# Performance work log

Hardware: AMD Instinct MI355X
Metric: run time of the kernel (lower is better)

## Reference

```python
import jax, jax.numpy as jnp
import numpy as np

VOXEL_SIZE = (0.2, 0.2, 4.0)
BN_EPS = 1e-3
N_PILLARS, MAX_PTS, IN_CH, OUT_CH = 100000, 32, 4, 64


def setup_inputs() -> dict:
    key = jax.random.key(0)
    k0, k1, k2, k3, k4 = jax.random.split(key, 5)
    features = jax.random.normal(k0, (N_PILLARS, MAX_PTS, IN_CH), dtype=jnp.float32)
    num_points = jax.random.randint(k1, (N_PILLARS,), 1, MAX_PTS + 1).astype(jnp.int32)
    batch = jax.random.randint(k2, (N_PILLARS, 1), 0, 4)
    z = jnp.zeros((N_PILLARS, 1), dtype=jnp.int32)
    yx = jax.random.randint(k3, (N_PILLARS, 2), 0, 512)
    coors = jnp.concatenate([batch, z, yx], axis=1).astype(jnp.int32)  # (b, z, y, x)
    # PFN params: Linear(10 -> 64, no bias, kaiming), BN affine
    W = jax.random.normal(k4, (IN_CH + 6, OUT_CH), dtype=jnp.float32) * np.sqrt(2.0 / (IN_CH + 6))
    gamma = jnp.ones((OUT_CH,), dtype=jnp.float32)
    beta = jnp.zeros((OUT_CH,), dtype=jnp.float32)
    return {"features": features, "W": W, "gamma": gamma, "beta": beta,
            "num_points": num_points, "coors": coors}


def reference(features, W, gamma, beta, num_points, coors):
    # features: [N, P, 4]; coors: [N, 4] (batch, z, y, x)
    vs = jnp.asarray(VOXEL_SIZE, dtype=features.dtype)
    P = features.shape[1]
    xyz = features[..., :3]  # [N, P, 3]
    # padding indicator: point j of pillar i is valid iff j < num_points[i]
    maskf = (jnp.arange(P)[None, :] < num_points[:, None]).astype(features.dtype)[..., None]  # [N,P,1]
    # cluster center: masked mean of xyz per pillar, broadcast back to points
    cnt = jnp.maximum(num_points, 1).astype(features.dtype)[:, None]
    voxel_mean = (xyz * maskf).sum(axis=1) / cnt  # [N, 3]
    f_cluster = xyz - voxel_mean[:, None, :]
    # voxel center offset (faithful to source: coors[:, 1:] * voxel_size + 0.5*voxel_size)
    voxel_center = (coors[:, 1:].astype(features.dtype) + 0.5) * vs  # [N, 3]
    f_center = xyz - voxel_center[:, None, :]
    feats = jnp.concatenate([features, f_cluster, f_center], axis=-1) * maskf  # [N, P, 10]
    # PFN layer: Linear -> BatchNorm (training stats over all points, per channel) -> ReLU
    h = jnp.einsum('npc,cd->npd', feats, W)  # [N, P, 64]
    mu = h.mean(axis=(0, 1))
    var = h.var(axis=(0, 1))
    h = (h - mu) * jax.lax.rsqrt(var + BN_EPS) * gamma + beta
    h = jax.nn.relu(h)
    # dynamic_scatter with mode='max': max-reduce points within each pillar
    voxel_feats = h.max(axis=1)  # [N, 64]
    return voxel_feats
```

## Files before the change

kernel.cpp:

```cpp
#include <hip/hip_runtime.h>
#include <stdint.h>

#define NP 100000
#define MP 32
#define OC 64
#define NBLK 1563
#define BNEPS 0.001f
#define MTOT 3200000.0
#define GIDX(i,j) ((i)*10 - (i)*((i)-1)/2 + ((j)-(i)))
#define BG(a,b) B[((a)<=(b)) ? ((a)*(7-(a))/2+(b)) : ((b)*(7-(b))/2+(a))]

typedef float f2 __attribute__((ext_vector_type(2)));

__device__ __forceinline__ float redall(float v) {
    v += __int_as_float(__builtin_amdgcn_update_dpp(0, __float_as_int(v), 0xB1,  0xF, 0xF, true));
    v += __int_as_float(__builtin_amdgcn_update_dpp(0, __float_as_int(v), 0x4E,  0xF, 0xF, true));
    v += __int_as_float(__builtin_amdgcn_update_dpp(0, __float_as_int(v), 0x141, 0xF, 0xF, true));
    v += __int_as_float(__builtin_amdgcn_update_dpp(0, __float_as_int(v), 0x140, 0xF, 0xF, true));
    v += __int_as_float(__builtin_amdgcn_ds_swizzle(__float_as_int(v), 0x401F));
    v += __shfl_xor(v, 32, 64);
    return v;
}

__global__ void sap_prep(const float* __restrict__ W, const float* __restrict__ gamma,
                         float* __restrict__ wptab, float4* __restrict__ btab)
{
    const int c = threadIdx.x;
    float w2[4], wcl[3], wce[3];
    w2[3] = W[3 * OC + c];
    #pragma unroll
    for (int k = 0; k < 3; ++k) {
        wcl[k] = W[(4 + k) * OC + c];
        wce[k] = W[(7 + k) * OC + c];
        w2[k]  = W[k * OC + c] + wcl[k] + wce[k];
    }
    const float sgn = (gamma[c] >= 0.0f) ? 1.0f : -1.0f;
    #pragma unroll
    for (int k = 0; k < 4; ++k)
        wptab[(((c >> 1) * 4) + k) * 2 + (c & 1)] = w2[k] * sgn;
    btab[2*c]   = make_float4(wcl[0]*sgn, wcl[1]*sgn, wcl[2]*sgn, wce[0]*sgn);
    btab[2*c+1] = make_float4(wce[1]*sgn, wce[2]*sgn, sgn, 0.0f);
}

__global__ __launch_bounds__(256, 4) void sap_pass1(
    const float4* __restrict__ feat4, const int* __restrict__ nump,
    const int4* __restrict__ coors4, const f2* __restrict__ wptab,
    const float4* __restrict__ btab, float* __restrict__ hsel,
    float* __restrict__ partials)
{
    const int lane = threadIdx.x & 63;
    const int swid = __builtin_amdgcn_readfirstlane(threadIdx.x >> 6);
    const int n = blockIdx.x * 64 + lane;
    const bool valid = n < NP;
    const int nn = valid ? n : NP - 1;
    const int cnt = valid ? nump[nn] : 0;
    const int4 cr = coors4[nn];
    const float cenz = ((float)cr.y + 0.5f) * 0.2f;
    const float ceny = ((float)cr.z + 0.5f) * 0.2f;
    const float cenx = ((float)cr.w + 0.5f) * 4.0f;
    const float4* __restrict__ fp = feat4 + (size_t)nn * MP;

    f2 wA[8], wB[8], wC[8], wD[8];
    #pragma unroll
    for (int j = 0; j < 8; ++j) {
        const int base = (swid * 8 + j) * 4;
        wA[j] = wptab[base];     wB[j] = wptab[base + 1];
        wC[j] = wptab[base + 2]; wD[j] = wptab[base + 3];
    }

    f2 mac[8];
    #pragma unroll
    for (int j = 0; j < 8; ++j) mac[j] = (f2){-3.0e38f, -3.0e38f};
    float S0 = 0.f, S1 = 0.f, S2 = 0.f, S3 = 0.f;
    float B[10];
    #pragma unroll
    for (int k = 0; k < 10; ++k) B[k] = 0.f;
    const bool doB = (swid == 0);

#define POINT(FF, P) {                                                          \
    const bool act = (P) < cnt;                                                 \
    const float neg = act ? 0.0f : -3.0e38f;                                    \
    const f2 neg2 = {neg, neg};                                                 \
    const f2 fx = {(FF).x, (FF).x}, fy = {(FF).y, (FF).y};                      \
    const f2 fz = {(FF).z, (FF).z}, fw = {(FF).w, (FF).w};                      \
    _Pragma("unroll")                                                           \
    for (int j = 0; j < 8; ++j) {                                               \
        const f2 d = __builtin_elementwise_fma(fx, wA[j],                       \
                     __builtin_elementwise_fma(fy, wB[j],                       \
                     __builtin_elementwise_fma(fz, wC[j],                       \
                     __builtin_elementwise_fma(fw, wD[j], neg2))));             \
        mac[j] = __builtin_elementwise_max(mac[j], d);                          \
    }                                                                           \
    const float ax = act ? (FF).x : 0.0f, ay = act ? (FF).y : 0.0f;             \
    const float az = act ? (FF).z : 0.0f;                                       \
    S0 += ax; S1 += ay; S2 += az;                                               \
    if (doB) {                                                                  \
        const float aw = act ? (FF).w : 0.0f;                                   \
        S3 += aw;                                                               \
        B[0]=fmaf(ax,ax,B[0]); B[1]=fmaf(ax,ay,B[1]); B[2]=fmaf(ax,az,B[2]);    \
        B[3]=fmaf(ax,aw,B[3]); B[4]=fmaf(ay,ay,B[4]); B[5]=fmaf(ay,az,B[5]);    \
        B[6]=fmaf(ay,aw,B[6]); B[7]=fmaf(az,az,B[7]); B[8]=fmaf(az,aw,B[8]);    \
        B[9]=fmaf(aw,aw,B[9]);                                                  \
    } }

    {
        float4 b0 = fp[0], b1 = fp[1], b2 = fp[2], b3 = fp[3];
        #pragma unroll 1
        for (int pq = 0; pq < 8; ++pq) {
            const int pb = pq * 4;
            float4 n0 = b0, n1 = b1, n2 = b2, n3 = b3;
            if (pq < 7) { n0 = fp[pb+4]; n1 = fp[pb+5]; n2 = fp[pb+6]; n3 = fp[pb+7]; }
            POINT(b0, pb + 0) POINT(b1, pb + 1)
            POINT(b2, pb + 2) POINT(b3, pb + 3)
            b0 = n0; b1 = n1; b2 = n2; b3 = n3;
        }
    }
#undef POINT

    const float fcnt = (float)cnt;
    const float rc = __builtin_amdgcn_rcpf(fmaxf(fcnt, 1.0f));
    const float mx = S0 * rc, my = S1 * rc, mz = S2 * rc;
    const float fl = (cnt < MP) ? 0.0f : -3.0e38f;
    #pragma unroll
    for (int q = 0; q < 4; ++q) {
        float o[4];
        #pragma unroll
        for (int k = 0; k < 4; ++k) {
            const int cc = q * 4 + k;
            const int c = swid * 16 + cc;
            const float4 bA = btab[2 * c];
            const float4 bB = btab[2 * c + 1];
            const float bias = -(mx * bA.x + my * bA.y + mz * bA.z
                               + cenz * bA.w + ceny * bB.x + cenx * bB.y);
            const float m = (cc & 1) ? mac[cc >> 1].y : mac[cc >> 1].x;
            o[k] = bB.z * fmaxf(m + bias, fl);
        }
        if (valid)
            *reinterpret_cast<float4*>(hsel + (size_t)n * OC + swid * 16 + q * 4)
                = make_float4(o[0], o[1], o[2], o[3]);
    }

    if (doB) {
        float vals[62];
        const float Sf[4] = {S0, S1, S2, S3};
        const float mu[3] = {S0 * rc, S1 * rc, S2 * rc};
        const float ce[3] = {cenz, ceny, cenx};
        #pragma unroll
        for (int i = 0; i < 4; ++i)
            #pragma unroll
            for (int j = i; j < 4; ++j)
                vals[GIDX(i, j)] = BG(i, j);
        #pragma unroll
        for (int i = 0; i < 4; ++i)
            #pragma unroll
            for (int t = 0; t < 3; ++t)
                vals[GIDX(i, 4 + t)] = BG(i, t) - mu[t] * Sf[i];
        #pragma unroll
        for (int s = 0; s < 3; ++s)
            #pragma unroll
            for (int t = s; t < 3; ++t)
                vals[GIDX(4 + s, 4 + t)] = BG(s, t) - mu[s] * Sf[t];
        #pragma unroll
        for (int i = 0; i < 4; ++i)
            #pragma unroll
            for (int t = 0; t < 3; ++t)
                vals[GIDX(i, 7 + t)] = BG(i, t) - ce[t] * Sf[i];
        #pragma unroll
        for (int s = 0; s < 3; ++s)
            #pragma unroll
            for (int t = 0; t < 3; ++t)
                vals[GIDX(4 + s, 7 + t)] = BG(s, t) - mu[s] * Sf[t];
        #pragma unroll
        for (int s = 0; s < 3; ++s)
            #pragma unroll
            for (int t = s; t < 3; ++t)
                vals[GIDX(7 + s, 7 + t)] =
                    fmaf(fcnt * ce[s], ce[t], BG(s, t) - ce[s] * Sf[t] - ce[t] * Sf[s]);
        vals[55] = S0; vals[56] = S1; vals[57] = S2; vals[58] = S3;
        vals[59] = fmaf(-fcnt, cenz, S0);
        vals[60] = fmaf(-fcnt, ceny, S1);
        vals[61] = fmaf(-fcnt, cenx, S2);

        #pragma unroll
        for (int k = 0; k < 62; ++k) vals[k] = redall(vals[k]);
        float mine = 0.0f;
        #pragma unroll
        for (int k = 0; k < 62; ++k) mine = (lane == k) ? vals[k] : mine;
        if (lane < 62)
            partials[(size_t)blockIdx.x * 64 + lane] = mine;
    }
}

__global__ __launch_bounds__(256) void sap_reduce1(const float* __restrict__ partials,
                                                   float* __restrict__ partials2)
{
    __shared__ float acc[4][64];
    const int k = threadIdx.x & 63, q = threadIdx.x >> 6;
    const int g = blockIdx.x;
    float s = 0.0f;
    for (int b = g + 64 * q; b < NBLK; b += 256)
        s += partials[(size_t)b * 64 + k];
    acc[q][k] = s;
    __syncthreads();
    if (threadIdx.x < 64)
        partials2[(size_t)g * 64 + threadIdx.x] =
            (acc[0][threadIdx.x] + acc[1][threadIdx.x]) +
            (acc[2][threadIdx.x] + acc[3][threadIdx.x]);
}

__global__ void sap_finalize(const float* __restrict__ partials2,
                             const float* __restrict__ W,
                             const float* __restrict__ gamma,
                             const float* __restrict__ beta,
                             float* __restrict__ scsh)
{
    __shared__ float acc[4][64];
    __shared__ float stats[64];
    const int tid = threadIdx.x;
    const int k = tid & 63, q = tid >> 6;
    float s = 0.0f;
    #pragma unroll
    for (int i = 0; i < 16; ++i)
        s += partials2[(size_t)(q + 4 * i) * 64 + k];
    acc[q][k] = s;
    __syncthreads();
    if (tid < 64) stats[tid] = (acc[0][tid] + acc[1][tid]) + (acc[2][tid] + acc[3][tid]);
    __syncthreads();
    if (tid >= 64) return;
    const int c = tid;
    double G[55];
    #pragma unroll
    for (int kk = 0; kk < 55; ++kk) G[kk] = (double)stats[kk];
    double Sg[10];
    Sg[0] = (double)stats[55]; Sg[1] = (double)stats[56];
    Sg[2] = (double)stats[57]; Sg[3] = (double)stats[58];
    Sg[4] = 0.0; Sg[5] = 0.0; Sg[6] = 0.0;
    Sg[7] = (double)stats[59]; Sg[8] = (double)stats[60]; Sg[9] = (double)stats[61];
    double w[10];
    #pragma unroll
    for (int kk = 0; kk < 10; ++kk) w[kk] = (double)W[kk * OC + c];
    double sh = 0.0, qq = 0.0;
    #pragma unroll
    for (int kk = 0; kk < 10; ++kk) sh += Sg[kk] * w[kk];
    for (int i = 0; i < 10; ++i)
        for (int j = i; j < 10; ++j) {
            const double t = w[i] * w[j] * G[GIDX(i, j)];
            qq += (i == j) ? t : 2.0 * t;
        }
    const double mu_d = sh / MTOT;
    const double var_d = qq / MTOT - mu_d * mu_d;
    const float sc = gamma[c] * rsqrtf((float)var_d + BNEPS);
    scsh[c]      = sc;
    scsh[64 + c] = beta[c] - (float)mu_d * sc;
}

__global__ __launch_bounds__(256) void sap_pass2(const float* __restrict__ scsh,
                                                 float* __restrict__ out)
{
    const int idx = blockIdx.x * 256 + threadIdx.x;
    if (idx >= (NP * OC) / 4) return;
    float4 h = reinterpret_cast<float4*>(out)[idx];
    const int ci = idx & 15;
    const float4 sc = reinterpret_cast<const float4*>(scsh)[ci];
    const float4 sh = reinterpret_cast<const float4*>(scsh + 64)[ci];
    float4 o;
    o.x = fmaxf(fmaf(h.x, sc.x, sh.x), 0.0f);
    o.y = fmaxf(fmaf(h.y, sc.y, sh.y), 0.0f);
    o.z = fmaxf(fmaf(h.z, sc.z, sh.z), 0.0f);
    o.w = fmaxf(fmaf(h.w, sc.w, sh.w), 0.0f);
    reinterpret_cast<float4*>(out)[idx] = o;
}

extern "C" void kernel_launch(void* const* d_in, const int* in_sizes, int n_in,
                              void* d_out, int out_size, void* d_ws, size_t ws_size,
                              hipStream_t stream) {
    const float* feat  = (const float*)d_in[0];
    const float* W     = (const float*)d_in[1];
    const float* gamma = (const float*)d_in[2];
    const float* beta  = (const float*)d_in[3];
    const int*   nump  = (const int*)d_in[4];
    const int*   coors = (const int*)d_in[5];
    float* out = (float*)d_out;

    float* wptab = (float*)d_ws;
    float4* btab = (float4*)((char*)d_ws + 1024);
    float* scsh  = (float*)((char*)d_ws + 3072);
    float* partials  = (float*)((char*)d_ws + 4096);
    float* partials2 = (float*)((char*)d_ws + 4096 + 1563*64*4);

    sap_prep<<<1, 64, 0, stream>>>(W, gamma, wptab, btab);
    sap_pass1<<<NBLK, 256, 0, stream>>>(
        (const float4*)feat, nump, (const int4*)coors, (const f2*)wptab,
        btab, out, partials);
    sap_reduce1<<<64, 256, 0, stream>>>(partials, partials2);
    sap_finalize<<<1, 256, 0, stream>>>(partials2, W, gamma, beta, scsh);
    sap_pass2<<<(NP * OC / 4 + 255) / 256, 256, 0, stream>>>(scsh, out);
}
```

Before: 60.57 us.

## Stage pillar features into LDS via direct global-to-LDS loads with XOR swizzle

Each block cooperatively copies its 64 pillars' point features into shared memory using direct global-to-LDS loads with a swizzled layout, then every wave reads points from LDS instead of global memory. This removes the fourfold redundant global/L1 traffic from the four waves processing the same pillars. It costs 32KB of LDS per block, adds a block barrier, and drops the previous register prefetch overlap of loads with compute.

```diff
diff --git a/kernel.cpp b/kernel.cpp
--- a/kernel.cpp
+++ b/kernel.cpp
@@ -11,6 +11,8 @@
 #define BG(a,b) B[((a)<=(b)) ? ((a)*(7-(a))/2+(b)) : ((b)*(7-(b))/2+(a))]
 
 typedef float f2 __attribute__((ext_vector_type(2)));
+typedef __attribute__((address_space(3))) uint32_t as3_u32;
+typedef const __attribute__((address_space(1))) uint32_t as1_u32;
 
 __device__ __forceinline__ float redall(float v) {
     v += __int_as_float(__builtin_amdgcn_update_dpp(0, __float_as_int(v), 0xB1,  0xF, 0xF, true));
@@ -48,8 +50,24 @@
     const float4* __restrict__ btab, float* __restrict__ hsel,
     float* __restrict__ partials)
 {
-    const int lane = threadIdx.x & 63;
-    const int swid = __builtin_amdgcn_readfirstlane(threadIdx.x >> 6);
+    __shared__ float lds[64 * MP * 4];
+    const int tid  = threadIdx.x;
+    const int lane = tid & 63;
+    const int swid = __builtin_amdgcn_readfirstlane(tid >> 6);
+
+    {
+        const size_t blockBase = (size_t)blockIdx.x * (64 * MP);
+        #pragma unroll
+        for (int it = 0; it < 8; ++it) {
+            const int g = it * 256 + tid;
+            const int pil = g >> 5, pg = g & 31;
+            size_t se = blockBase + (size_t)(pil * MP + (pg ^ (pil & 31)));
+            if (se >= (size_t)NP * MP) se = 0;
+            __builtin_amdgcn_global_load_lds((as1_u32*)(feat4 + se),
+                                             (as3_u32*)(&lds[g * 4]), 16, 0, 0);
+        }
+    }
+
     const int n = blockIdx.x * 64 + lane;
     const bool valid = n < NP;
     const int nn = valid ? n : NP - 1;
@@ -58,7 +76,6 @@
     const float cenz = ((float)cr.y + 0.5f) * 0.2f;
     const float ceny = ((float)cr.z + 0.5f) * 0.2f;
     const float cenx = ((float)cr.w + 0.5f) * 4.0f;
-    const float4* __restrict__ fp = feat4 + (size_t)nn * MP;
 
     f2 wA[8], wB[8], wC[8], wD[8];
     #pragma unroll
@@ -76,6 +93,12 @@
     #pragma unroll
     for (int k = 0; k < 10; ++k) B[k] = 0.f;
     const bool doB = (swid == 0);
+
+    __syncthreads();
+
+    const float4* __restrict__ lp = reinterpret_cast<const float4*>(lds);
+    const int gb = lane << 5;
+    const int xm = lane & 31;
 
 #define POINT(FF, P) {                                                          \
     const bool act = (P) < cnt;                                                 \
@@ -104,15 +127,15 @@
     } }
 
     {
-        float4 b0 = fp[0], b1 = fp[1], b2 = fp[2], b3 = fp[3];
         #pragma unroll 1
         for (int pq = 0; pq < 8; ++pq) {
             const int pb = pq * 4;
-            float4 n0 = b0, n1 = b1, n2 = b2, n3 = b3;
-            if (pq < 7) { n0 = fp[pb+4]; n1 = fp[pb+5]; n2 = fp[pb+6]; n3 = fp[pb+7]; }
-            POINT(b0, pb + 0) POINT(b1, pb + 1)
-            POINT(b2, pb + 2) POINT(b3, pb + 3)
-            b0 = n0; b1 = n1; b2 = n2; b3 = n3;
+            const float4 f0 = lp[gb + ((pb + 0) ^ xm)];
+            const float4 f1 = lp[gb + ((pb + 1) ^ xm)];
+            const float4 f2v = lp[gb + ((pb + 2) ^ xm)];
+            const float4 f3 = lp[gb + ((pb + 3) ^ xm)];
+            POINT(f0, pb + 0) POINT(f1, pb + 1)
+            POINT(f2v, pb + 2) POINT(f3, pb + 3)
         }
     }
 #undef POINT
```

Result: faster. 58.65 us (-3.2%).
